# Kernel optimization log

Hardware: AMD Instinct MI355X
Metric: run time of the kernel (lower is better)

## Reference

```python
import jax, jax.numpy as jnp
import numpy as np

B, S, D, H = 2, 2048, 1024, 16
HD = D // H
EPS = 1e-5


def layer_norm(x, g, b):
    mu = jnp.mean(x, axis=-1, keepdims=True)
    var = jnp.mean(jnp.square(x - mu), axis=-1, keepdims=True)
    return (x - mu) * jax.lax.rsqrt(var + EPS) * g + b


def setup_inputs() -> dict:
    key = jax.random.key(0)
    ks = jax.random.split(key, 10)
    x = jax.random.normal(ks[0], (B, S, D), dtype=jnp.float32)
    # pad the tail 256 key positions (True = masked), no fully-masked causal rows
    padding_mask = jnp.broadcast_to(jnp.arange(S) >= (S - 256), (B, S))
    std = 0.02
    return {
        "x": x,
        "padding_mask": padding_mask,
        "qkv_w": jax.random.normal(ks[1], (D, 3 * D), dtype=jnp.float32) * std,
        "qkv_b": jnp.zeros((3 * D,), jnp.float32),
        "out_w": jax.random.normal(ks[2], (D, D), dtype=jnp.float32) * std,
        "out_b": jnp.zeros((D,), jnp.float32),
        "attn_ln_g": jnp.ones((D,), jnp.float32),
        "attn_ln_b": jnp.zeros((D,), jnp.float32),
        "ff1_w": jax.random.normal(ks[3], (D, 4 * D), dtype=jnp.float32) * std,
        "ff1_b": jnp.zeros((4 * D,), jnp.float32),
        "ff2_w": jax.random.normal(ks[4], (4 * D, D), dtype=jnp.float32) * std,
        "ff2_b": jnp.zeros((D,), jnp.float32),
        "ff_ln_g": jnp.ones((D,), jnp.float32),
        "ff_ln_b": jnp.zeros((D,), jnp.float32),
    }


def reference(x, padding_mask, qkv_w, qkv_b, out_w, out_b, attn_ln_g, attn_ln_b,
              ff1_w, ff1_b, ff2_w, ff2_b, ff_ln_g, ff_ln_b):
    b, s, d = x.shape
    neg_inf = jnp.finfo(x.dtype).min
    # --- pre-norm self-attention (dropout=0 / eval) ---
    h = layer_norm(x, attn_ln_g, attn_ln_b)
    qkv = h @ qkv_w + qkv_b                       # [B,S,3D]
    q, k, v = jnp.split(qkv, 3, axis=-1)
    q = q.reshape(b, s, H, HD).transpose(0, 2, 1, 3)  # [B,H,S,hd]
    k = k.reshape(b, s, H, HD).transpose(0, 2, 1, 3)
    v = v.reshape(b, s, H, HD).transpose(0, 2, 1, 3)
    w = jnp.einsum('bhqd,bhkd->bhqk', q, k) / np.sqrt(HD).astype(x.dtype)
    causal = jnp.triu(jnp.ones((s, s), dtype=bool), 1)          # future mask
    mask = causal[None, None] | padding_mask[:, None, None, :]  # [B,1,S,S]
    w = jnp.where(mask, neg_inf, w)
    w = jax.nn.softmax(w, axis=-1)
    attn = jnp.einsum('bhqk,bhkd->bhqd', w, v)
    attn = attn.transpose(0, 2, 1, 3).reshape(b, s, d)
    attn = attn @ out_w + out_b
    x = x + attn
    # --- pre-norm FFN with exact (erf) GELU ---
    h = layer_norm(x, ff_ln_g, ff_ln_b)
    h = jax.nn.gelu(h @ ff1_w + ff1_b, approximate=False)
    h = h @ ff2_w + ff2_b
    x = x + h
    return x
```

## Files before the change

### kernel.cpp

```cpp
#include <hip/hip_runtime.h>


typedef unsigned short ushort_t;
typedef __bf16 bf16x8 __attribute__((ext_vector_type(8)));
typedef float  f32x4  __attribute__((ext_vector_type(4)));
typedef float  f32x16 __attribute__((ext_vector_type(16)));
typedef int    i32x4  __attribute__((ext_vector_type(4)));
typedef int    i32x2  __attribute__((ext_vector_type(2)));

#define LOG2E 1.44269504f

__device__ __forceinline__ ushort_t f2bf_bits(float f) {
  unsigned u = __builtin_bit_cast(unsigned, f);
  u += 0x7fffu + ((u >> 16) & 1u);
  return (ushort_t)(u >> 16);
}
__device__ __forceinline__ unsigned pack2(float lo, float hi) {
  return (unsigned)f2bf_bits(lo) | ((unsigned)f2bf_bits(hi) << 16);
}
__device__ __forceinline__ bf16x8 ld_bf8(const ushort_t* p) {
  return __builtin_bit_cast(bf16x8, *(const i32x4*)(p));
}
__device__ __forceinline__ void gload16(const void* g, void* l) {
  __builtin_amdgcn_global_load_lds(
      (const __attribute__((address_space(1))) void*)g,
      (__attribute__((address_space(3))) void*)l, 16, 0, 0);
}
__device__ __forceinline__ void make_pfrags(const f32x16& p, bf16x8& f0, bf16x8& f1) {
  unsigned w0 = pack2(p[0], p[1]), w1 = pack2(p[2], p[3]);
  unsigned w2 = pack2(p[4], p[5]), w3 = pack2(p[6], p[7]);
  unsigned w4 = pack2(p[8], p[9]), w5 = pack2(p[10], p[11]);
  unsigned w6 = pack2(p[12], p[13]), w7 = pack2(p[14], p[15]);
  const i32x2 s02 = __builtin_amdgcn_permlane32_swap((int)w0, (int)w2, false, false);
  const i32x2 s13 = __builtin_amdgcn_permlane32_swap((int)w1, (int)w3, false, false);
  const i32x2 s46 = __builtin_amdgcn_permlane32_swap((int)w4, (int)w6, false, false);
  const i32x2 s57 = __builtin_amdgcn_permlane32_swap((int)w5, (int)w7, false, false);
  i32x4 a, b;
  a[0] = s02[0]; a[1] = s13[0]; a[2] = s02[1]; a[3] = s13[1];
  b[0] = s46[0]; b[1] = s57[0]; b[2] = s46[1]; b[3] = s57[1];
  f0 = __builtin_bit_cast(bf16x8, a);
  f1 = __builtin_bit_cast(bf16x8, b);
}

__global__ __launch_bounds__(256)
void wt_kernel(const float* __restrict__ w, ushort_t* __restrict__ wt, int K, int N) {
  __shared__ float tile[32][33];
  const int tx = threadIdx.x, ty = threadIdx.y;
  const int n0 = blockIdx.x << 5, k0 = blockIdx.y << 5;
#pragma unroll
  for (int i = 0; i < 4; ++i)
    tile[ty + i * 8][tx] = w[(size_t)(k0 + ty + i * 8) * N + n0 + tx];
  __syncthreads();
#pragma unroll
  for (int i = 0; i < 4; ++i)
    wt[(size_t)(n0 + ty + i * 8) * K + k0 + tx] = f2bf_bits(tile[tx][ty + i * 8]);
}

__global__ __launch_bounds__(256)
void vt_kernel(const ushort_t* __restrict__ v, ushort_t* __restrict__ vt) {
  __shared__ ushort_t tile[32][33];
  const int tx = threadIdx.x, ty = threadIdx.y;
  const int d0 = blockIdx.x << 5, s0 = blockIdx.y << 5, bh = blockIdx.z;
  const ushort_t* vp = v + (size_t)bh * (2048 * 64);
  ushort_t* vtp = vt + (size_t)bh * (64 * 2048);
#pragma unroll
  for (int i = 0; i < 4; ++i)
    tile[ty + i * 8][tx] = vp[(size_t)(s0 + ty + i * 8) * 64 + d0 + tx];
  __syncthreads();
#pragma unroll
  for (int i = 0; i < 4; ++i)
    vtp[(size_t)(d0 + ty + i * 8) * 2048 + s0 + tx] = tile[tx][ty + i * 8];
}

__global__ __launch_bounds__(256)
void ln_kernel(const float* __restrict__ x, const float* __restrict__ gw,
               const float* __restrict__ bw, ushort_t* __restrict__ out) {
  const int row = blockIdx.x, t = threadIdx.x;
  const float4 v = ((const float4*)(x + (size_t)row * 1024))[t];
  float s = v.x + v.y + v.z + v.w;
  float s2 = v.x * v.x + v.y * v.y + v.z * v.z + v.w * v.w;
#pragma unroll
  for (int off = 32; off >= 1; off >>= 1) {
    s += __shfl_xor(s, off);
    s2 += __shfl_xor(s2, off);
  }
  __shared__ float red[8];
  if ((t & 63) == 0) { red[t >> 6] = s; red[4 + (t >> 6)] = s2; }
  __syncthreads();
  const float fs = red[0] + red[1] + red[2] + red[3];
  const float fs2 = red[4] + red[5] + red[6] + red[7];
  const float mu = fs * 0.0009765625f;
  const float var = fs2 * 0.0009765625f - mu * mu;
  const float rs = rsqrtf(var + 1e-5f);
  const float4 gg = ((const float4*)gw)[t];
  const float4 bb = ((const float4*)bw)[t];
  ushort4 o;
  o.x = f2bf_bits((v.x - mu) * rs * gg.x + bb.x);
  o.y = f2bf_bits((v.y - mu) * rs * gg.y + bb.y);
  o.z = f2bf_bits((v.z - mu) * rs * gg.z + bb.z);
  o.w = f2bf_bits((v.w - mu) * rs * gg.w + bb.w);
  ((ushort4*)(out + (size_t)row * 1024))[t] = o;
}

enum { EPI_QKV = 0, EPI_RESID = 1, EPI_GELU = 2 };

template <int EPI>
__global__ __launch_bounds__(256)
void gemm_bt(const ushort_t* __restrict__ A, const ushort_t* __restrict__ Bt,
             const float* __restrict__ bias,
             const float* res, float* outf,
             ushort_t* __restrict__ outb,
             ushort_t* __restrict__ qo, ushort_t* __restrict__ ko, ushort_t* __restrict__ vo,
             int M, int N, int K) {
  __shared__ __align__(16) char smem[32768];
  const int tid = threadIdx.x;
  const int lane = tid & 63;
  const int wv = tid >> 6, wm = wv >> 1, wn = wv & 1;
  const int nbx = N >> 7;
  const int nsx = nbx >> 3;
  const int cpx = gridDim.x >> 3;
  const int swz = (blockIdx.x & 7) * cpx + (blockIdx.x >> 3);
  const int st = swz >> 6, wi = swz & 63;
  const int m0 = (((st / nsx) << 3) + (wi >> 3)) << 7;
  const int n0 = (((st % nsx) << 3) + (wi & 7)) << 7;
  const int l15 = lane & 15, g = lane >> 4;
  const int coloff = ((g ^ ((lane >> 1) & 3)) << 4);

  const int slo = tid, shi = tid + 256;
  const int rlo = slo >> 2, klo = (((slo & 3) ^ ((rlo >> 1) & 3)) << 3);
  const int rhi = shi >> 2, khi = (((shi & 3) ^ ((rhi >> 1) & 3)) << 3);
  const ushort_t* Aglo = A + (size_t)(m0 + rlo) * K + klo;
  const ushort_t* Aghi = A + (size_t)(m0 + rhi) * K + khi;
  const ushort_t* Bglo = Bt + (size_t)(n0 + rlo) * K + klo;
  const ushort_t* Bghi = Bt + (size_t)(n0 + rhi) * K + khi;

  auto stage = [&](int buf, int kt) {
    char* base = smem + (buf << 14);
    gload16(Aglo + kt, base + slo * 16);
    gload16(Aghi + kt, base + shi * 16);
    gload16(Bglo + kt, base + 8192 + slo * 16);
    gload16(Bghi + kt, base + 8192 + shi * 16);
  };

  f32x4 acc[4][4];
#pragma unroll
  for (int m = 0; m < 4; ++m)
#pragma unroll
    for (int n = 0; n < 4; ++n) acc[m][n] = (f32x4){0.f, 0.f, 0.f, 0.f};

  stage(0, 0);
  int cur = 0;
  for (int kt = 0; kt < K; kt += 32) {
    if (kt + 32 < K) {
      stage(cur ^ 1, kt + 32);
      asm volatile("s_waitcnt vmcnt(4)" ::: "memory");
    } else {
      asm volatile("s_waitcnt vmcnt(0)" ::: "memory");
    }
    __builtin_amdgcn_s_barrier();
    const char* ldsA = smem + (cur << 14);
    const char* ldsB = ldsA + 8192;
    bf16x8 af[4], bfv[4];
#pragma unroll
    for (int m = 0; m < 4; ++m)
      af[m] = __builtin_bit_cast(
          bf16x8, *(const i32x4*)(ldsA + ((wm << 6) + (m << 4) + l15) * 64 + coloff));
#pragma unroll
    for (int n = 0; n < 4; ++n)
      bfv[n] = __builtin_bit_cast(
          bf16x8, *(const i32x4*)(ldsB + ((wn << 6) + (n << 4) + l15) * 64 + coloff));
#pragma unroll
    for (int m = 0; m < 4; ++m)
#pragma unroll
      for (int n = 0; n < 4; ++n)
        acc[m][n] = __builtin_amdgcn_mfma_f32_16x16x32_bf16(af[m], bfv[n], acc[m][n], 0, 0, 0);
    __builtin_amdgcn_s_barrier();
    cur ^= 1;
  }

#pragma unroll
  for (int m = 0; m < 4; ++m) {
#pragma unroll
    for (int n = 0; n < 4; ++n) {
#pragma unroll
      for (int r = 0; r < 4; ++r) {
        const int grow = m0 + (wm << 6) + (m << 4) + (g << 2) + r;
        const int gcol = n0 + (wn << 6) + (n << 4) + l15;
        float v = acc[m][n][r] + bias[gcol];
        if (EPI == EPI_RESID) {
          outf[(size_t)grow * N + gcol] = v + res[(size_t)grow * N + gcol];
        } else if (EPI == EPI_GELU) {
          const float gl = 0.5f * v * (1.0f + erff(v * 0.70710678118f));
          outb[(size_t)grow * N + gcol] = f2bf_bits(gl);
        } else {
          const int part = gcol >> 10, within = gcol & 1023;
          const int hh = within >> 6, dd = within & 63;
          const int bb = grow >> 11, ss = grow & 2047;
          if (part == 0) v *= 0.125f;
          ushort_t* dst = (part == 0) ? qo : ((part == 1) ? ko : vo);
          dst[((size_t)(bb * 16 + hh) * 2048 + ss) * 64 + dd] = f2bf_bits(v);
        }
      }
    }
  }
}

__global__ __launch_bounds__(256)
void attnc_kernel(const ushort_t* __restrict__ qb, const ushort_t* __restrict__ kb,
                  const ushort_t* __restrict__ vtb, ushort_t* __restrict__ attn) {
  __shared__ __align__(16) char smem[32768];
  const int tid = threadIdx.x;
  const int lane = tid & 63, wv = tid >> 6;
  const int bx = blockIdx.x;
  const int xcd = bx & 7, c = bx >> 3;
  const int bhl = (((c >> 5) & 1) << 1) | ((c >> 4) & 1);
  const int qblk = ((c >> 5) & 1) ? (15 - (c & 15)) : (c & 15);
  const int bh = (xcd << 2) + bhl;
  const int q0b = qblk << 7;
  const int l31 = lane & 31, h32 = lane >> 5;
  const int qs = q0b + (wv << 5);

  const ushort_t* kbase = kb + (size_t)bh * (2048 * 64);
  const ushort_t* vbase = vtb + (size_t)bh * (64 * 2048);
  const ushort_t* qp = qb + (size_t)bh * (2048 * 64);

  bf16x8 qf[4];
#pragma unroll
  for (int t = 0; t < 4; ++t)
    qf[t] = ld_bf8(qp + (size_t)(qs + l31) * 64 + t * 16 + h32 * 8);

  f32x16 o0, o1;
#pragma unroll
  for (int i = 0; i < 16; ++i) { o0[i] = 0.f; o1[i] = 0.f; }
  float mrun = -1e30f, lrun = 0.f;

  const int kmaxq = (q0b + 127 < 1791) ? (q0b + 127) : 1791;
  const int nkb = (kmaxq >> 6) + 1;

  auto stage = [&](int buf, int k0) {
#pragma unroll
    for (int c2 = 0; c2 < 2; ++c2) {
      const int slot = (c2 << 8) + tid;
      const int row = slot >> 3;
      const int jj = (slot & 7) ^ (row & 7);
      char* dK = smem + buf * 16384 + slot * 16;
      gload16(kbase + (size_t)(k0 + row) * 64 + jj * 8, dK);
      gload16(vbase + (size_t)row * 2048 + k0 + jj * 8, dK + 8192);
    }
  };

  stage(0, 0);
  __syncthreads();
  int cur = 0;

  for (int blk = 0; blk < nkb; ++blk) {
    const int k0 = blk << 6;
    if (blk + 1 < nkb) stage(cur ^ 1, (blk + 1) << 6);

    if (k0 <= qs) {
      const char* bK = smem + cur * 16384;
      const char* bV = bK + 8192;
      const bool a1 = (k0 + 32 <= qs);

      f32x16 st0;
#pragma unroll
      for (int i = 0; i < 16; ++i) st0[i] = 0.f;
#pragma unroll
      for (int t = 0; t < 4; ++t) {
        const int r = l31, j = t * 2 + h32;
        const bf16x8 kf = ld_bf8((const ushort_t*)(bK + r * 128 + ((j ^ (r & 7)) << 4)));
        st0 = __builtin_amdgcn_mfma_f32_32x32x16_bf16(kf, qf[t], st0, 0, 0, 0);
      }
      if (k0 == qs) {
#pragma unroll
        for (int r = 0; r < 16; ++r) {
          const int klocal = (r & 3) + ((r >> 2) << 3) + (h32 << 2);
          st0[r] = (klocal <= l31) ? st0[r] : -1e30f;
        }
      }
      f32x16 st1;
      if (a1) {
#pragma unroll
        for (int i = 0; i < 16; ++i) st1[i] = 0.f;
#pragma unroll
        for (int t = 0; t < 4; ++t) {
          const int r = 32 + l31, j = t * 2 + h32;
          const bf16x8 kf = ld_bf8((const ushort_t*)(bK + r * 128 + ((j ^ (r & 7)) << 4)));
          st1 = __builtin_amdgcn_mfma_f32_32x32x16_bf16(kf, qf[t], st1, 0, 0, 0);
        }
        if (k0 + 32 == qs) {
#pragma unroll
          for (int r = 0; r < 16; ++r) {
            const int klocal = (r & 3) + ((r >> 2) << 3) + (h32 << 2);
            st1[r] = (klocal <= l31) ? st1[r] : -1e30f;
          }
        }
      }

      float bmax = st0[0];
#pragma unroll
      for (int r = 1; r < 16; ++r) bmax = fmaxf(bmax, st0[r]);
      if (a1) {
#pragma unroll
        for (int r = 0; r < 16; ++r) bmax = fmaxf(bmax, st1[r]);
      }
      bmax = fmaxf(bmax, __shfl_xor(bmax, 32));

      if (!__all(bmax <= mrun + 8.0f)) {
        const float mnew = fmaxf(mrun, bmax);
        const float alpha = exp2f((mrun - mnew) * LOG2E);
        lrun *= alpha;
        o0 *= alpha;
        o1 *= alpha;
        mrun = mnew;
      }
      const float nm = -mrun * LOG2E;
      float sum = 0.f;
#pragma unroll
      for (int r = 0; r < 16; ++r) {
        st0[r] = exp2f(fmaf(st0[r], LOG2E, nm));
        sum += st0[r];
      }
      if (a1) {
#pragma unroll
        for (int r = 0; r < 16; ++r) {
          st1[r] = exp2f(fmaf(st1[r], LOG2E, nm));
          sum += st1[r];
        }
      }
      sum += __shfl_xor(sum, 32);
      lrun += sum;

      bf16x8 f0, f1, f2, f3;
      make_pfrags(st0, f0, f1);
      if (a1) make_pfrags(st1, f2, f3);

      const int r0 = l31, r1 = 32 + l31;
      const bf16x8 v00 = ld_bf8((const ushort_t*)(bV + r0 * 128 + (((h32) ^ (r0 & 7)) << 4)));
      const bf16x8 v01 = ld_bf8((const ushort_t*)(bV + r0 * 128 + (((2 + h32) ^ (r0 & 7)) << 4)));
      const bf16x8 v10 = ld_bf8((const ushort_t*)(bV + r1 * 128 + (((h32) ^ (r1 & 7)) << 4)));
      const bf16x8 v11 = ld_bf8((const ushort_t*)(bV + r1 * 128 + (((2 + h32) ^ (r1 & 7)) << 4)));
      o0 = __builtin_amdgcn_mfma_f32_32x32x16_bf16(v00, f0, o0, 0, 0, 0);
      o0 = __builtin_amdgcn_mfma_f32_32x32x16_bf16(v01, f1, o0, 0, 0, 0);
      o1 = __builtin_amdgcn_mfma_f32_32x32x16_bf16(v10, f0, o1, 0, 0, 0);
      o1 = __builtin_amdgcn_mfma_f32_32x32x16_bf16(v11, f1, o1, 0, 0, 0);
      if (a1) {
        const bf16x8 v02 = ld_bf8((const ushort_t*)(bV + r0 * 128 + (((4 + h32) ^ (r0 & 7)) << 4)));
        const bf16x8 v03 = ld_bf8((const ushort_t*)(bV + r0 * 128 + (((6 + h32) ^ (r0 & 7)) << 4)));
        const bf16x8 v12 = ld_bf8((const ushort_t*)(bV + r1 * 128 + (((4 + h32) ^ (r1 & 7)) << 4)));
        const bf16x8 v13 = ld_bf8((const ushort_t*)(bV + r1 * 128 + (((6 + h32) ^ (r1 & 7)) << 4)));
        o0 = __builtin_amdgcn_mfma_f32_32x32x16_bf16(v02, f2, o0, 0, 0, 0);
        o0 = __builtin_amdgcn_mfma_f32_32x32x16_bf16(v03, f3, o0, 0, 0, 0);
        o1 = __builtin_amdgcn_mfma_f32_32x32x16_bf16(v12, f2, o1, 0, 0, 0);
        o1 = __builtin_amdgcn_mfma_f32_32x32x16_bf16(v13, f3, o1, 0, 0, 0);
      }
    }
    __syncthreads();
    cur ^= 1;
  }

  const float inv = 1.f / lrun;
  ushort_t* elds = (ushort_t*)smem + wv * 2112;
#pragma unroll
  for (int r = 0; r < 16; ++r) {
    const int d = (r & 3) + ((r >> 2) << 3) + (h32 << 2);
    elds[d * 33 + l31] = f2bf_bits(o0[r] * inv);
    elds[(d + 32) * 33 + l31] = f2bf_bits(o1[r] * inv);
  }
  __syncthreads();
  const int b = bh >> 4, h = bh & 15;
  ushort_t tmp[32];
#pragma unroll
  for (int e = 0; e < 32; ++e) tmp[e] = elds[(h32 * 32 + e) * 33 + l31];
  ushort_t* op = attn + (size_t)((b << 11) + qs + l31) * 1024 + (h << 6) + h32 * 32;
#pragma unroll
  for (int c4 = 0; c4 < 4; ++c4)
    *(i32x4*)(op + c4 * 8) = *(const i32x4*)(tmp + c4 * 8);
}

extern "C" void kernel_launch(void* const* d_in, const int* in_sizes, int n_in,
                              void* d_out, int out_size, void* d_ws, size_t ws_size,
                              hipStream_t stream) {
  const float* x      = (const float*)d_in[0];
  const float* qkv_w  = (const float*)d_in[2];
  const float* qkv_b  = (const float*)d_in[3];
  const float* out_w  = (const float*)d_in[4];
  const float* out_b  = (const float*)d_in[5];
  const float* ln1g   = (const float*)d_in[6];
  const float* ln1b   = (const float*)d_in[7];
  const float* ff1_w  = (const float*)d_in[8];
  const float* ff1_b  = (const float*)d_in[9];
  const float* ff2_w  = (const float*)d_in[10];
  const float* ff2_b  = (const float*)d_in[11];
  const float* ln2g   = (const float*)d_in[12];
  const float* ln2b   = (const float*)d_in[13];

  char* ws = (char*)d_ws;
  ushort_t* wqkvT = (ushort_t*)(ws + 0);
  ushort_t* woutT = (ushort_t*)(ws + 6291456);
  ushort_t* wff1T = (ushort_t*)(ws + 8388608);
  ushort_t* wff2T = (ushort_t*)(ws + 16777216);
  ushort_t* hbuf  = (ushort_t*)(ws + 25165824);
  ushort_t* qbuf  = (ushort_t*)(ws + 33554432);
  ushort_t* kbuf  = (ushort_t*)(ws + 41943040);
  ushort_t* vbuf  = (ushort_t*)(ws + 50331648);
  ushort_t* vtbuf = (ushort_t*)(ws + 58720256);
  ushort_t* ff1o  = kbuf;
  float* x1 = (float*)d_out;

  const dim3 tb(32, 8);
  wt_kernel<<<dim3(96, 32), tb, 0, stream>>>(qkv_w, wqkvT, 1024, 3072);
  wt_kernel<<<dim3(32, 32), tb, 0, stream>>>(out_w, woutT, 1024, 1024);
  wt_kernel<<<dim3(128, 32), tb, 0, stream>>>(ff1_w, wff1T, 1024, 4096);
  wt_kernel<<<dim3(32, 128), tb, 0, stream>>>(ff2_w, wff2T, 4096, 1024);

  ln_kernel<<<4096, 256, 0, stream>>>(x, ln1g, ln1b, hbuf);

  gemm_bt<EPI_QKV><<<24 * 32, 256, 0, stream>>>(
      hbuf, wqkvT, qkv_b, nullptr, nullptr, nullptr, qbuf, kbuf, vbuf, 4096, 3072, 1024);

  vt_kernel<<<dim3(2, 64, 32), tb, 0, stream>>>(vbuf, vtbuf);

  attnc_kernel<<<512, 256, 0, stream>>>(qbuf, kbuf, vtbuf, hbuf);

  gemm_bt<EPI_RESID><<<8 * 32, 256, 0, stream>>>(
      hbuf, woutT, out_b, x, x1, nullptr, nullptr, nullptr, nullptr, 4096, 1024, 1024);

  ln_kernel<<<4096, 256, 0, stream>>>(x1, ln2g, ln2b, qbuf);

  gemm_bt<EPI_GELU><<<32 * 32, 256, 0, stream>>>(
      qbuf, wff1T, ff1_b, nullptr, nullptr, ff1o, nullptr, nullptr, nullptr, 4096, 4096, 1024);

  gemm_bt<EPI_RESID><<<8 * 32, 256, 0, stream>>>(
      ff1o, wff2T, ff2_b, x1, x1, nullptr, nullptr, nullptr, nullptr, 4096, 1024, 4096);
}
```

Before: 279.6 us.

## Generalize GEMM to 8-wave blocks with larger tiles and 64-wide K steps

Replaces the fixed 128x128, 4-wave GEMM with a templated 8-wave kernel that uses 256x256 tiles for the QKV and FF1 GEMMs and 128x128 tiles for the output and FF2 projections. The K step grows from 32 to 64, which halves the number of barriers, and LDS uses a 128-byte-row XOR swizzle. Larger tiles raise arithmetic intensity and data reuse per block. In exchange they add register pressure, since 256x256 tiles give 32 accumulators per wave, and they reduce the block count, which can hurt load balance across CUs. The 256x256 QKV GEMM launches only 192 blocks.

New measurement: 295.1 us. +5.5%, slower.

```diff
diff --git a/kernel.cpp b/kernel.cpp
--- a/kernel.cpp
+++ b/kernel.cpp
@@ -104,88 +104,112 @@
 
 enum { EPI_QKV = 0, EPI_RESID = 1, EPI_GELU = 2 };
 
-template <int EPI>
-__global__ __launch_bounds__(256)
-void gemm_bt(const ushort_t* __restrict__ A, const ushort_t* __restrict__ Bt,
-             const float* __restrict__ bias,
-             const float* res, float* outf,
-             ushort_t* __restrict__ outb,
-             ushort_t* __restrict__ qo, ushort_t* __restrict__ ko, ushort_t* __restrict__ vo,
-             int M, int N, int K) {
-  __shared__ __align__(16) char smem[32768];
+template <int BM, int BN, int EPI>
+__global__ __launch_bounds__(512, 2)
+void gemm8(const ushort_t* __restrict__ A, const ushort_t* __restrict__ Bt,
+           const float* __restrict__ bias,
+           const float* res, float* outf,
+           ushort_t* __restrict__ outb,
+           ushort_t* __restrict__ qo, ushort_t* __restrict__ ko, ushort_t* __restrict__ vo,
+           int M, int N, int K) {
+  constexpr int ABYTES = BM * 128;
+  constexpr int BBYTES = BN * 128;
+  constexpr int TILEB = ABYTES + BBYTES;
+  constexpr int MR = BM / 32;
+  constexpr int NR = BN / 64;
+  constexpr int AI = BM / 64;
+  constexpr int BI = BN / 64;
+  constexpr int LPS = AI + BI;
+  __shared__ __align__(16) char smem[2 * TILEB];
+
   const int tid = threadIdx.x;
   const int lane = tid & 63;
-  const int wv = tid >> 6, wm = wv >> 1, wn = wv & 1;
-  const int nbx = N >> 7;
-  const int nsx = nbx >> 3;
+  const int wv = tid >> 6, wm = wv >> 2, wn = wv & 3;
+  const int l15 = lane & 15, g = lane >> 4;
+
+  const int nbx = N / BN, nby = M / BM;
   const int cpx = gridDim.x >> 3;
   const int swz = (blockIdx.x & 7) * cpx + (blockIdx.x >> 3);
-  const int st = swz >> 6, wi = swz & 63;
-  const int m0 = (((st / nsx) << 3) + (wi >> 3)) << 7;
-  const int n0 = (((st % nsx) << 3) + (wi & 7)) << 7;
-  const int l15 = lane & 15, g = lane >> 4;
-  const int coloff = ((g ^ ((lane >> 1) & 3)) << 4);
-
-  const int slo = tid, shi = tid + 256;
-  const int rlo = slo >> 2, klo = (((slo & 3) ^ ((rlo >> 1) & 3)) << 3);
-  const int rhi = shi >> 2, khi = (((shi & 3) ^ ((rhi >> 1) & 3)) << 3);
-  const ushort_t* Aglo = A + (size_t)(m0 + rlo) * K + klo;
-  const ushort_t* Aghi = A + (size_t)(m0 + rhi) * K + khi;
-  const ushort_t* Bglo = Bt + (size_t)(n0 + rlo) * K + klo;
-  const ushort_t* Bghi = Bt + (size_t)(n0 + rhi) * K + khi;
+  int m0, n0;
+  if ((nbx & 7) == 0 && (nby & 7) == 0) {
+    const int nsx = nbx >> 3;
+    const int st = swz >> 6, wi = swz & 63;
+    m0 = ((st / nsx) * 8 + (wi >> 3)) * BM;
+    n0 = ((st % nsx) * 8 + (wi & 7)) * BN;
+  } else {
+    m0 = (swz / nbx) * BM;
+    n0 = (swz % nbx) * BN;
+  }
 
   auto stage = [&](int buf, int kt) {
-    char* base = smem + (buf << 14);
-    gload16(Aglo + kt, base + slo * 16);
-    gload16(Aghi + kt, base + shi * 16);
-    gload16(Bglo + kt, base + 8192 + slo * 16);
-    gload16(Bghi + kt, base + 8192 + shi * 16);
+    char* base = smem + buf * TILEB;
+#pragma unroll
+    for (int i = 0; i < AI; ++i) {
+      const int s = tid + (i << 9);
+      const int row = s >> 3, j = (s & 7) ^ (row & 7);
+      gload16(A + (size_t)(m0 + row) * K + kt + (j << 3), base + s * 16);
+    }
+#pragma unroll
+    for (int i = 0; i < BI; ++i) {
+      const int s = tid + (i << 9);
+      const int row = s >> 3, j = (s & 7) ^ (row & 7);
+      gload16(Bt + (size_t)(n0 + row) * K + kt + (j << 3), base + ABYTES + s * 16);
+    }
   };
 
-  f32x4 acc[4][4];
-#pragma unroll
-  for (int m = 0; m < 4; ++m)
-#pragma unroll
-    for (int n = 0; n < 4; ++n) acc[m][n] = (f32x4){0.f, 0.f, 0.f, 0.f};
+  f32x4 acc[MR][NR];
+#pragma unroll
+  for (int m = 0; m < MR; ++m)
+#pragma unroll
+    for (int n = 0; n < NR; ++n) acc[m][n] = (f32x4){0.f, 0.f, 0.f, 0.f};
 
   stage(0, 0);
   int cur = 0;
-  for (int kt = 0; kt < K; kt += 32) {
-    if (kt + 32 < K) {
-      stage(cur ^ 1, kt + 32);
-      asm volatile("s_waitcnt vmcnt(4)" ::: "memory");
+  for (int kt = 0; kt < K; kt += 64) {
+    if (kt + 64 < K) {
+      stage(cur ^ 1, kt + 64);
+      if constexpr (LPS == 8)
+        asm volatile("s_waitcnt vmcnt(8)" ::: "memory");
+      else
+        asm volatile("s_waitcnt vmcnt(4)" ::: "memory");
     } else {
       asm volatile("s_waitcnt vmcnt(0)" ::: "memory");
     }
     __builtin_amdgcn_s_barrier();
-    const char* ldsA = smem + (cur << 14);
-    const char* ldsB = ldsA + 8192;
-    bf16x8 af[4], bfv[4];
-#pragma unroll
-    for (int m = 0; m < 4; ++m)
-      af[m] = __builtin_bit_cast(
-          bf16x8, *(const i32x4*)(ldsA + ((wm << 6) + (m << 4) + l15) * 64 + coloff));
-#pragma unroll
-    for (int n = 0; n < 4; ++n)
-      bfv[n] = __builtin_bit_cast(
-          bf16x8, *(const i32x4*)(ldsB + ((wn << 6) + (n << 4) + l15) * 64 + coloff));
-#pragma unroll
-    for (int m = 0; m < 4; ++m)
-#pragma unroll
-      for (int n = 0; n < 4; ++n)
-        acc[m][n] = __builtin_amdgcn_mfma_f32_16x16x32_bf16(af[m], bfv[n], acc[m][n], 0, 0, 0);
+    const char* bA = smem + cur * TILEB;
+    const char* bB = bA + ABYTES;
+#pragma unroll
+    for (int kk = 0; kk < 2; ++kk) {
+      const int jb = (kk << 2) + g;
+      bf16x8 af[MR], bfr[NR];
+#pragma unroll
+      for (int m = 0; m < MR; ++m) {
+        const int r = wm * (BM / 2) + (m << 4) + l15;
+        af[m] = ld_bf8((const ushort_t*)(bA + r * 128 + ((jb ^ (r & 7)) << 4)));
+      }
+#pragma unroll
+      for (int n = 0; n < NR; ++n) {
+        const int r = wn * (BN / 4) + (n << 4) + l15;
+        bfr[n] = ld_bf8((const ushort_t*)(bB + r * 128 + ((jb ^ (r & 7)) << 4)));
+      }
+#pragma unroll
+      for (int m = 0; m < MR; ++m)
+#pragma unroll
+        for (int n = 0; n < NR; ++n)
+          acc[m][n] = __builtin_amdgcn_mfma_f32_16x16x32_bf16(af[m], bfr[n], acc[m][n], 0, 0, 0);
+    }
     __builtin_amdgcn_s_barrier();
     cur ^= 1;
   }
 
 #pragma unroll
-  for (int m = 0; m < 4; ++m) {
-#pragma unroll
-    for (int n = 0; n < 4; ++n) {
+  for (int m = 0; m < MR; ++m) {
+#pragma unroll
+    for (int n = 0; n < NR; ++n) {
 #pragma unroll
       for (int r = 0; r < 4; ++r) {
-        const int grow = m0 + (wm << 6) + (m << 4) + (g << 2) + r;
-        const int gcol = n0 + (wn << 6) + (n << 4) + l15;
+        const int grow = m0 + wm * (BM / 2) + (m << 4) + (g << 2) + r;
+        const int gcol = n0 + wn * (BN / 4) + (n << 4) + l15;
         float v = acc[m][n][r] + bias[gcol];
         if (EPI == EPI_RESID) {
           outf[(size_t)grow * N + gcol] = v + res[(size_t)grow * N + gcol];
@@ -416,21 +440,21 @@
 
   ln_kernel<<<4096, 256, 0, stream>>>(x, ln1g, ln1b, hbuf);
 
-  gemm_bt<EPI_QKV><<<24 * 32, 256, 0, stream>>>(
+  gemm8<256, 256, EPI_QKV><<<192, 512, 0, stream>>>(
       hbuf, wqkvT, qkv_b, nullptr, nullptr, nullptr, qbuf, kbuf, vbuf, 4096, 3072, 1024);
 
   vt_kernel<<<dim3(2, 64, 32), tb, 0, stream>>>(vbuf, vtbuf);
 
   attnc_kernel<<<512, 256, 0, stream>>>(qbuf, kbuf, vtbuf, hbuf);
 
-  gemm_bt<EPI_RESID><<<8 * 32, 256, 0, stream>>>(
+  gemm8<128, 128, EPI_RESID><<<256, 512, 0, stream>>>(
       hbuf, woutT, out_b, x, x1, nullptr, nullptr, nullptr, nullptr, 4096, 1024, 1024);
 
   ln_kernel<<<4096, 256, 0, stream>>>(x1, ln2g, ln2b, qbuf);
 
-  gemm_bt<EPI_GELU><<<32 * 32, 256, 0, stream>>>(
+  gemm8<256, 256, EPI_GELU><<<256, 512, 0, stream>>>(
       qbuf, wff1T, ff1_b, nullptr, nullptr, ff1o, nullptr, nullptr, nullptr, 4096, 4096, 1024);
 
-  gemm_bt<EPI_RESID><<<8 * 32, 256, 0, stream>>>(
+  gemm8<128, 128, EPI_RESID><<<256, 512, 0, stream>>>(
       ff1o, wff2T, ff2_b, x1, x1, nullptr, nullptr, nullptr, nullptr, 4096, 1024, 4096);
 }
```

## Add 256x256-tile 8-wave GEMM with phased staging for QKV and FF1

Applied to the files above, without the earlier changes.

Introduces a new GEMM kernel using 256x256 output tiles, 512 threads and 128KB LDS double-buffering, with the next K-tile staged in four quarter-phases interleaved with MFMA work and priority bumps. It replaces the 128x128 GEMM for the QKV projection and FF1+GELU, aiming for more data reuse per LDS load and better overlap of global loads with compute. The old GEMM gains a fallback tile mapping for grids not divisible by 8. The risk is lower occupancy and fewer blocks (192 for QKV) than CUs, which leaves part of the device idle.

After: 326.1 us. +16.6%, slower.

```diff
diff --git a/kernel.cpp b/kernel.cpp
--- a/kernel.cpp
+++ b/kernel.cpp
@@ -105,6 +105,133 @@
 enum { EPI_QKV = 0, EPI_RESID = 1, EPI_GELU = 2 };
 
 template <int EPI>
+__global__ __launch_bounds__(512, 2)
+void gemm4p(const ushort_t* __restrict__ A, const ushort_t* __restrict__ Bt,
+            const float* __restrict__ bias,
+            const float* res, float* outf,
+            ushort_t* __restrict__ outb,
+            ushort_t* __restrict__ qo, ushort_t* __restrict__ ko, ushort_t* __restrict__ vo,
+            int M, int N, int K) {
+  __shared__ __align__(16) char smem[131072];
+  const int tid = threadIdx.x;
+  const int lane = tid & 63;
+  const int wv = tid >> 6, wm = wv >> 2, wn = wv & 3;
+  const int l15 = lane & 15, g = lane >> 4;
+
+  const int nbx = N >> 8, nby = M >> 8;
+  const int cpx = gridDim.x >> 3;
+  const int swz = (blockIdx.x & 7) * cpx + (blockIdx.x >> 3);
+  int m0, n0;
+  if ((nbx & 7) == 0 && (nby & 7) == 0) {
+    const int nsx = nbx >> 3;
+    const int st = swz >> 6, wi = swz & 63;
+    m0 = (((st / nsx) << 3) + (wi >> 3)) << 8;
+    n0 = (((st % nsx) << 3) + (wi & 7)) << 8;
+  } else {
+    m0 = (swz / nbx) << 8;
+    n0 = (swz % nbx) << 8;
+  }
+
+  auto stageh = [&](int buf, int kt, int hh) {
+    const ushort_t* src = (hh < 2) ? A : Bt;
+    const int rbase = ((hh < 2) ? m0 : n0) + ((hh & 1) << 7);
+    char* base = smem + (buf << 16) + (hh << 14);
+#pragma unroll
+    for (int i = 0; i < 2; ++i) {
+      const int s = tid + (i << 9);
+      const int row = s >> 3, j = (s & 7) ^ (row & 7);
+      gload16(src + (size_t)(rbase + row) * K + kt + (j << 3), base + s * 16);
+    }
+  };
+
+  f32x4 acc[8][4];
+#pragma unroll
+  for (int m = 0; m < 8; ++m)
+#pragma unroll
+    for (int n = 0; n < 4; ++n) acc[m][n] = (f32x4){0.f, 0.f, 0.f, 0.f};
+
+  stageh(0, 0, 0); stageh(0, 0, 1); stageh(0, 0, 2); stageh(0, 0, 3);
+  int cur = 0;
+  for (int kt = 0; kt < K; kt += 64) {
+    const char* bufb = smem + (cur << 16);
+    const int nxt = cur ^ 1, ktn = kt + 64;
+    const bool last = (ktn >= K);
+    if (!last) {
+      stageh(nxt, ktn, 0);
+      asm volatile("s_waitcnt vmcnt(2)" ::: "memory");
+    } else {
+      asm volatile("s_waitcnt vmcnt(0)" ::: "memory");
+    }
+    __builtin_amdgcn_s_barrier();
+    __builtin_amdgcn_sched_barrier(0);
+#pragma unroll
+    for (int p = 0; p < 4; ++p) {
+      const int mh = p >> 1, nh = p & 1;
+      bf16x8 af[2][4], bfv[2][2];
+#pragma unroll
+      for (int kk = 0; kk < 2; ++kk) {
+        const int jb = (kk << 2) + g;
+#pragma unroll
+        for (int m = 0; m < 4; ++m) {
+          const int r = (wm << 7) + (mh << 6) + (m << 4) + l15;
+          af[kk][m] = ld_bf8((const ushort_t*)(bufb + ((r >> 7) << 14) +
+                                               ((r & 127) << 7) + ((jb ^ (r & 7)) << 4)));
+        }
+#pragma unroll
+        for (int n = 0; n < 2; ++n) {
+          const int r = (wn << 6) + (nh << 5) + (n << 4) + l15;
+          bfv[kk][n] = ld_bf8((const ushort_t*)(bufb + 32768 + ((r >> 7) << 14) +
+                                                ((r & 127) << 7) + ((jb ^ (r & 7)) << 4)));
+        }
+      }
+      if (!last && p < 3) stageh(nxt, ktn, p + 1);
+      __builtin_amdgcn_s_barrier();
+      __builtin_amdgcn_sched_barrier(0);
+      __builtin_amdgcn_s_setprio(1);
+#pragma unroll
+      for (int kk = 0; kk < 2; ++kk)
+#pragma unroll
+        for (int m = 0; m < 4; ++m)
+#pragma unroll
+          for (int n = 0; n < 2; ++n)
+            acc[(mh << 2) + m][(nh << 1) + n] = __builtin_amdgcn_mfma_f32_16x16x32_bf16(
+                af[kk][m], bfv[kk][n], acc[(mh << 2) + m][(nh << 1) + n], 0, 0, 0);
+      __builtin_amdgcn_s_setprio(0);
+      if (p == 3) asm volatile("s_waitcnt lgkmcnt(0)" ::: "memory");
+      __builtin_amdgcn_sched_barrier(0);
+      __builtin_amdgcn_s_barrier();
+    }
+    cur ^= 1;
+  }
+
+#pragma unroll
+  for (int am = 0; am < 8; ++am) {
+#pragma unroll
+    for (int an = 0; an < 4; ++an) {
+#pragma unroll
+      for (int r = 0; r < 4; ++r) {
+        const int grow = m0 + (wm << 7) + ((am >> 2) << 6) + ((am & 3) << 4) + (g << 2) + r;
+        const int gcol = n0 + (wn << 6) + ((an >> 1) << 5) + ((an & 1) << 4) + l15;
+        float v = acc[am][an][r] + bias[gcol];
+        if (EPI == EPI_RESID) {
+          outf[(size_t)grow * N + gcol] = v + res[(size_t)grow * N + gcol];
+        } else if (EPI == EPI_GELU) {
+          const float gl = 0.5f * v * (1.0f + erff(v * 0.70710678118f));
+          outb[(size_t)grow * N + gcol] = f2bf_bits(gl);
+        } else {
+          const int part = gcol >> 10, within = gcol & 1023;
+          const int hh = within >> 6, dd = within & 63;
+          const int bb = grow >> 11, ss = grow & 2047;
+          if (part == 0) v *= 0.125f;
+          ushort_t* dst = (part == 0) ? qo : ((part == 1) ? ko : vo);
+          dst[((size_t)(bb * 16 + hh) * 2048 + ss) * 64 + dd] = f2bf_bits(v);
+        }
+      }
+    }
+  }
+}
+
+template <int EPI>
 __global__ __launch_bounds__(256)
 void gemm_bt(const ushort_t* __restrict__ A, const ushort_t* __restrict__ Bt,
              const float* __restrict__ bias,
@@ -120,9 +247,15 @@
   const int nsx = nbx >> 3;
   const int cpx = gridDim.x >> 3;
   const int swz = (blockIdx.x & 7) * cpx + (blockIdx.x >> 3);
-  const int st = swz >> 6, wi = swz & 63;
-  const int m0 = (((st / nsx) << 3) + (wi >> 3)) << 7;
-  const int n0 = (((st % nsx) << 3) + (wi & 7)) << 7;
+  int m0, n0;
+  if (nsx > 0) {
+    const int st = swz >> 6, wi = swz & 63;
+    m0 = (((st / nsx) << 3) + (wi >> 3)) << 7;
+    n0 = (((st % nsx) << 3) + (wi & 7)) << 7;
+  } else {
+    m0 = (swz / nbx) << 7;
+    n0 = (swz % nbx) << 7;
+  }
   const int l15 = lane & 15, g = lane >> 4;
   const int coloff = ((g ^ ((lane >> 1) & 3)) << 4);
 
@@ -416,21 +549,21 @@
 
   ln_kernel<<<4096, 256, 0, stream>>>(x, ln1g, ln1b, hbuf);
 
-  gemm_bt<EPI_QKV><<<24 * 32, 256, 0, stream>>>(
+  gemm4p<EPI_QKV><<<192, 512, 0, stream>>>(
       hbuf, wqkvT, qkv_b, nullptr, nullptr, nullptr, qbuf, kbuf, vbuf, 4096, 3072, 1024);
 
   vt_kernel<<<dim3(2, 64, 32), tb, 0, stream>>>(vbuf, vtbuf);
 
   attnc_kernel<<<512, 256, 0, stream>>>(qbuf, kbuf, vtbuf, hbuf);
 
-  gemm_bt<EPI_RESID><<<8 * 32, 256, 0, stream>>>(
+  gemm_bt<EPI_RESID><<<256, 256, 0, stream>>>(
       hbuf, woutT, out_b, x, x1, nullptr, nullptr, nullptr, nullptr, 4096, 1024, 1024);
 
   ln_kernel<<<4096, 256, 0, stream>>>(x1, ln2g, ln2b, qbuf);
 
-  gemm_bt<EPI_GELU><<<32 * 32, 256, 0, stream>>>(
+  gemm4p<EPI_GELU><<<256, 512, 0, stream>>>(
       qbuf, wff1T, ff1_b, nullptr, nullptr, ff1o, nullptr, nullptr, nullptr, 4096, 4096, 1024);
 
-  gemm_bt<EPI_RESID><<<8 * 32, 256, 0, stream>>>(
+  gemm_bt<EPI_RESID><<<256, 256, 0, stream>>>(
       ff1o, wff2T, ff2_b, x1, x1, nullptr, nullptr, nullptr, nullptr, 4096, 1024, 4096);
 }
```
